# Kernel tuning notes

Hardware: AMD Instinct MI355X
Metric: run time of the kernel (lower is better)

The kernel has to match this reference:

```python
import jax, jax.numpy as jnp
import numpy as np

B, C, S, H, NC = 256, 2000, 50, 64, 3


def setup_inputs() -> dict:
    key = jax.random.key(0)
    ks = jax.random.split(key, 7)
    s = 1.0 / np.sqrt(H)  # PyTorch LSTM init scale
    return {
        "x": jax.random.normal(ks[0], (B, C, S), dtype=jnp.float32),
        "W_ih": jax.random.uniform(ks[1], (4 * H, 1), jnp.float32, -s, s),
        "W_hh": jax.random.uniform(ks[2], (4 * H, H), jnp.float32, -s, s),
        "b_ih": jax.random.uniform(ks[3], (4 * H,), jnp.float32, -s, s),
        "b_hh": jax.random.uniform(ks[4], (4 * H,), jnp.float32, -s, s),
        "W_fc": jax.random.uniform(ks[5], (NC, H), jnp.float32, -s, s),
        "b_fc": jax.random.uniform(ks[6], (NC,), jnp.float32, -s, s),
    }


def _lstm_last_h(x_flat, W_ih, W_hh, b_ih, b_hh):
    # x_flat: [N, S, 1] with N = B*C. PyTorch gate order: i, f, g, o.
    N = x_flat.shape[0]
    b = b_ih + b_hh  # [4H]
    # input_dim == 1, so precompute the input contribution for all steps:
    # [N, S, 1] @ [1, 4H] -> [N, S, 4H], then scan over time axis.
    x_proj = x_flat @ W_ih.T + b  # [N, S, 4H]
    xs = jnp.moveaxis(x_proj, 1, 0)  # [S, N, 4H]

    def step(carry, x_t):
        h, c = carry
        gates = x_t + h @ W_hh.T  # [N, 4H]
        i, f, g, o = jnp.split(gates, 4, axis=-1)
        i = jax.nn.sigmoid(i)
        f = jax.nn.sigmoid(f)
        g = jnp.tanh(g)
        o = jax.nn.sigmoid(o)
        c = f * c + i * g
        h = o * jnp.tanh(c)
        return (h, c), None

    h0 = jnp.zeros((N, x_proj.shape[-1] // 4), x_flat.dtype)
    (h_last, _), _ = jax.lax.scan(step, (h0, h0), xs)
    return h_last  # [N, H]


def reference(x, W_ih, W_hh, b_ih, b_hh, W_fc, b_fc):
    Bsz, Nc, Sl = x.shape
    x_flat = x.reshape(Bsz * Nc, Sl, 1)
    h_last = _lstm_last_h(x_flat, W_ih, W_hh, b_ih, b_hh)  # [B*C, H]
    logits = h_last @ W_fc.T + b_fc  # [B*C, NC]
    return logits.reshape(Bsz, Nc, -1)
```

## Files before the change

kernel.cpp:

```cpp
#include <hip/hip_runtime.h>

typedef _Float16 h4 __attribute__((ext_vector_type(4)));
typedef float f4 __attribute__((ext_vector_type(4)));

#define SEQ_LEN 50
#define HID 64
#define FSTRIDE 68

#if __has_builtin(__builtin_amdgcn_exp2f)
#define EXP2(x) __builtin_amdgcn_exp2f(x)
#else
extern "C" __device__ float __ocml_native_exp2_f32(float);
#define EXP2(x) __ocml_native_exp2_f32(x)
#endif
#define RCP(x) __builtin_amdgcn_rcpf(x)

#define MFMA16(A,B,C) __builtin_amdgcn_mfma_f32_16x16x16f16(A, B, C, 0, 0, 0)

#define LOG2E  1.442695041f
#define LOG2E2 2.885390082f

__global__ __launch_bounds__(256, 3)
void lstm_fused(const float* __restrict__ x,
                const float* __restrict__ W_ih,
                const float* __restrict__ W_hh,
                const float* __restrict__ b_ih,
                const float* __restrict__ b_hh,
                const float* __restrict__ W_fc,
                const float* __restrict__ b_fc,
                float* __restrict__ out)
{
    __shared__ h4    sW[16 * 4 * 64];
    __shared__ float sXT[SEQ_LEN * 64];

    const int tid  = threadIdx.x;
    const int wave = tid >> 6;
    const int lane = tid & 63;
    const int col  = lane & 15;
    const int quad = lane >> 4;
    const int seqBase = blockIdx.x << 6;

    for (int i = tid; i < SEQ_LEN * 64; i += 256) {
        const int s = i / SEQ_LEN;
        const int t = i - s * SEQ_LEN;
        sXT[t * 64 + s] = x[(size_t)(seqBase + s) * SEQ_LEN + t];
    }

    for (int i = tid; i < 16 * 4 * 64; i += 256) {
        const int ln   = i & 63;
        const int slot = (i >> 6) & 3;
        const int tile = i >> 8;
        const int gi = tile >> 2, dq = tile & 3;
        const int cl = ln & 15, qd = ln >> 4;
        const int n  = gi * 64 + dq * 16 + cl;
        const float scale = (gi == 2) ? LOG2E2 : LOG2E;
        h4 a = {};
        if (slot < 3) {
            const float* wp = W_hh + (size_t)n * HID + (slot + 1) * 16 + qd * 4;
            f4 w = *(const f4*)wp;
            a[0] = (_Float16)(w[0] * scale);
            a[1] = (_Float16)(w[1] * scale);
            a[2] = (_Float16)(w[2] * scale);
            a[3] = (_Float16)(w[3] * scale);
        } else if (qd == 0) {
            a[0] = (_Float16)(W_ih[n] * scale);
            a[1] = (_Float16)((b_ih[n] + b_hh[n]) * scale);
        }
        sW[(tile * 4 + slot) * 64 + ln] = a;
    }

    h4 Aw0[4][4];
    #pragma unroll
    for (int gi = 0; gi < 4; ++gi) {
        const float scale = (gi == 2) ? LOG2E2 : LOG2E;
        #pragma unroll
        for (int dq = 0; dq < 4; ++dq) {
            const int n = gi * 64 + dq * 16 + col;
            const float* wp = W_hh + (size_t)n * HID + quad * 4;
            f4 w = *(const f4*)wp;
            h4 a;
            a[0] = (_Float16)(w[0] * scale);
            a[1] = (_Float16)(w[1] * scale);
            a[2] = (_Float16)(w[2] * scale);
            a[3] = (_Float16)(w[3] * scale);
            Aw0[gi][dq] = a;
        }
    }

    const f4 z4 = {0.0f, 0.0f, 0.0f, 0.0f};

    h4 hB[4] = {};
    float c[4][4];
    #pragma unroll
    for (int dq = 0; dq < 4; ++dq)
        #pragma unroll
        for (int r = 0; r < 4; ++r) c[dq][r] = 0.0f;

    __syncthreads();

    #pragma clang loop unroll(disable)
    for (int t = 0; t < SEQ_LEN; ++t) {
        #pragma unroll
        for (int gi = 0; gi < 4; ++gi)
            #pragma unroll
            for (int dq = 0; dq < 4; ++dq)
                asm volatile("" : "+v"(Aw0[gi][dq]));
        int ob = lane;
        asm volatile("" : "+v"(ob));

        const float xt = sXT[t * 64 + wave * 16 + col];
        h4 bext = {};
        bext[0] = (_Float16)xt;
        bext[1] = (_Float16)1.0f;

        h4 hN[4];
        #pragma unroll
        for (int dq = 0; dq < 4; ++dq) {
            f4 acc[4];
            #pragma unroll
            for (int gi = 0; gi < 4; ++gi) {
                const int tb = (gi * 4 + dq) * 256;
                h4 ax = sW[tb + 3 * 64 + ob];
                h4 w1 = sW[tb + 0 * 64 + ob];
                h4 w2 = sW[tb + 1 * 64 + ob];
                h4 w3 = sW[tb + 2 * 64 + ob];
                f4 a = MFMA16(ax, bext, z4);
                a = MFMA16(Aw0[gi][dq], hB[0], a);
                a = MFMA16(w1, hB[1], a);
                a = MFMA16(w2, hB[2], a);
                a = MFMA16(w3, hB[3], a);
                acc[gi] = a;
            }
            h4 hv;
            #pragma unroll
            for (int rp = 0; rp < 2; ++rp) {
                const int r0 = rp * 2, r1 = r0 + 1;
                float EiA = EXP2(-acc[0][r0]);
                float EfA = EXP2(-acc[1][r0]);
                float EgA = EXP2( acc[2][r0]);
                float EoA = EXP2(-acc[3][r0]);
                float EiB = EXP2(-acc[0][r1]);
                float EfB = EXP2(-acc[1][r1]);
                float EgB = EXP2( acc[2][r1]);
                float EoB = EXP2(-acc[3][r1]);
                float piA = 1.0f + EiA, pfA = 1.0f + EfA;
                float pgA = 1.0f + EgA, poA = 1.0f + EoA;
                float piB = 1.0f + EiB, pfB = 1.0f + EfB;
                float pgB = 1.0f + EgB, poB = 1.0f + EoB;
                float t1A = piA * pgA,  t1B = piB * pgB;
                float DA  = pfA * t1A,  DB  = pfB * t1B;
                float vA  = fmaf(EgA, pfA, -pfA) * LOG2E2;
                float vB  = fmaf(EgB, pfB, -pfB) * LOG2E2;
                float numA = fmaf(c[dq][r0], t1A, vA);
                float numB = fmaf(c[dq][r1], t1B, vB);
                float R   = RCP(DA * DB);
                float cnA = fminf(numA * (R * DB), 40.0f);
                float cnB = fminf(numB * (R * DA), 40.0f);
                c[dq][r0] = cnA;
                c[dq][r1] = cnB;
                float EcA = EXP2(cnA), EcB = EXP2(cnB);
                float DhA = fmaf(poA, EcA, poA);
                float DhB = fmaf(poB, EcB, poB);
                float R2  = RCP(DhA * DhB);
                float rhA = R2 * DhB,  rhB = R2 * DhA;
                hv[r0] = (_Float16)fmaf(EcA, rhA, -rhA);
                hv[r1] = (_Float16)fmaf(EcB, rhB, -rhB);
            }
            hN[dq] = hv;
        }
        #pragma unroll
        for (int dq = 0; dq < 4; ++dq) hB[dq] = hN[dq];
    }

    __syncthreads();
    _Float16* sF = (_Float16*)sXT;
    #pragma unroll
    for (int dq = 0; dq < 4; ++dq)
        *(h4*)(sF + (wave * 16 + col) * FSTRIDE + dq * 16 + quad * 4) = hB[dq];

    if (lane < 48) {
        const int sl = lane / 3;
        const int nc = lane % 3;
        const _Float16* hp = sF + (wave * 16 + sl) * FSTRIDE;
        float a = b_fc[nc];
        #pragma unroll
        for (int u = 0; u < HID; ++u)
            a = fmaf((float)hp[u], W_fc[nc * HID + u], a);
        out[(size_t)(seqBase + wave * 16 + sl) * 3 + nc] = a;
    }
}

extern "C" void kernel_launch(void* const* d_in, const int* in_sizes, int n_in,
                              void* d_out, int out_size, void* d_ws, size_t ws_size,
                              hipStream_t stream) {
    const float* x    = (const float*)d_in[0];
    const float* W_ih = (const float*)d_in[1];
    const float* W_hh = (const float*)d_in[2];
    const float* b_ih = (const float*)d_in[3];
    const float* b_hh = (const float*)d_in[4];
    const float* W_fc = (const float*)d_in[5];
    const float* b_fc = (const float*)d_in[6];
    float* out = (float*)d_out;

    const int nSeq   = in_sizes[0] / SEQ_LEN;
    const int blocks = nSeq / 64;

    hipLaunchKernelGGL(lstm_fused, dim3(blocks), dim3(256), 0, stream,
                       x, W_ih, W_hh, b_ih, b_hh, W_fc, b_fc, out);
}
```

Measured before the change: 1.994 ms.

## Move second W_hh slice to registers and shrink LDS for higher occupancy

Keeps two of the four W_hh k-slices in registers instead of one, so each step reads only two weight fragments per tile from LDS. The input-projection weights become a packed 256-entry table masked per quad, and x is stored as fp16, which cuts LDS from about 45KB to about 23KB. Launch bounds go from 3 to 4 blocks per SIMD to raise occupancy. The final FC stage gets a rotated, unpadded read pattern to avoid bank conflicts. In exchange register pressure rises and could spill at the stricter occupancy target.

```diff
diff --git a/kernel.cpp b/kernel.cpp
--- a/kernel.cpp
+++ b/kernel.cpp
@@ -5,7 +5,6 @@
 
 #define SEQ_LEN 50
 #define HID 64
-#define FSTRIDE 68
 
 #if __has_builtin(__builtin_amdgcn_exp2f)
 #define EXP2(x) __builtin_amdgcn_exp2f(x)
@@ -20,7 +19,7 @@
 #define LOG2E  1.442695041f
 #define LOG2E2 2.885390082f
 
-__global__ __launch_bounds__(256, 3)
+__global__ __launch_bounds__(256, 4)
 void lstm_fused(const float* __restrict__ x,
                 const float* __restrict__ W_ih,
                 const float* __restrict__ W_hh,
@@ -30,8 +29,9 @@
                 const float* __restrict__ b_fc,
                 float* __restrict__ out)
 {
-    __shared__ h4    sW[16 * 4 * 64];
-    __shared__ float sXT[SEQ_LEN * 64];
+    __shared__ h4       sW[16 * 2 * 64];
+    __shared__ _Float16 sXh[SEQ_LEN * 64];
+    __shared__ unsigned sXpk[16 * 16];
 
     const int tid  = threadIdx.x;
     const int wave = tid >> 6;
@@ -43,33 +43,38 @@
     for (int i = tid; i < SEQ_LEN * 64; i += 256) {
         const int s = i / SEQ_LEN;
         const int t = i - s * SEQ_LEN;
-        sXT[t * 64 + s] = x[(size_t)(seqBase + s) * SEQ_LEN + t];
-    }
-
-    for (int i = tid; i < 16 * 4 * 64; i += 256) {
+        sXh[t * 64 + s] = (_Float16)x[(size_t)(seqBase + s) * SEQ_LEN + t];
+    }
+
+    for (int i = tid; i < 16 * 2 * 64; i += 256) {
         const int ln   = i & 63;
-        const int slot = (i >> 6) & 3;
-        const int tile = i >> 8;
+        const int s2   = (i >> 6) & 1;
+        const int tile = i >> 7;
         const int gi = tile >> 2, dq = tile & 3;
         const int cl = ln & 15, qd = ln >> 4;
         const int n  = gi * 64 + dq * 16 + cl;
         const float scale = (gi == 2) ? LOG2E2 : LOG2E;
-        h4 a = {};
-        if (slot < 3) {
-            const float* wp = W_hh + (size_t)n * HID + (slot + 1) * 16 + qd * 4;
-            f4 w = *(const f4*)wp;
-            a[0] = (_Float16)(w[0] * scale);
-            a[1] = (_Float16)(w[1] * scale);
-            a[2] = (_Float16)(w[2] * scale);
-            a[3] = (_Float16)(w[3] * scale);
-        } else if (qd == 0) {
-            a[0] = (_Float16)(W_ih[n] * scale);
-            a[1] = (_Float16)((b_ih[n] + b_hh[n]) * scale);
-        }
-        sW[(tile * 4 + slot) * 64 + ln] = a;
-    }
-
-    h4 Aw0[4][4];
+        const float* wp = W_hh + (size_t)n * HID + (s2 + 2) * 16 + qd * 4;
+        f4 w = *(const f4*)wp;
+        h4 a;
+        a[0] = (_Float16)(w[0] * scale);
+        a[1] = (_Float16)(w[1] * scale);
+        a[2] = (_Float16)(w[2] * scale);
+        a[3] = (_Float16)(w[3] * scale);
+        sW[i] = a;
+    }
+    if (tid < 256) {
+        const int cl = tid & 15, tile = tid >> 4;
+        const int gi = tile >> 2, dq = tile & 3;
+        const int n  = gi * 64 + dq * 16 + cl;
+        const float scale = (gi == 2) ? LOG2E2 : LOG2E;
+        union { _Float16 h[2]; unsigned u; } p;
+        p.h[0] = (_Float16)(W_ih[n] * scale);
+        p.h[1] = (_Float16)((b_ih[n] + b_hh[n]) * scale);
+        sXpk[tid] = p.u;
+    }
+
+    h4 Aw0[4][4], Aw1[4][4];
     #pragma unroll
     for (int gi = 0; gi < 4; ++gi) {
         const float scale = (gi == 2) ? LOG2E2 : LOG2E;
@@ -77,17 +82,20 @@
         for (int dq = 0; dq < 4; ++dq) {
             const int n = gi * 64 + dq * 16 + col;
             const float* wp = W_hh + (size_t)n * HID + quad * 4;
-            f4 w = *(const f4*)wp;
-            h4 a;
-            a[0] = (_Float16)(w[0] * scale);
-            a[1] = (_Float16)(w[1] * scale);
-            a[2] = (_Float16)(w[2] * scale);
-            a[3] = (_Float16)(w[3] * scale);
-            Aw0[gi][dq] = a;
+            f4 w0 = *(const f4*)wp;
+            f4 w1 = *(const f4*)(wp + 16);
+            h4 a0, a1;
+            a0[0] = (_Float16)(w0[0] * scale); a0[1] = (_Float16)(w0[1] * scale);
+            a0[2] = (_Float16)(w0[2] * scale); a0[3] = (_Float16)(w0[3] * scale);
+            a1[0] = (_Float16)(w1[0] * scale); a1[1] = (_Float16)(w1[1] * scale);
+            a1[2] = (_Float16)(w1[2] * scale); a1[3] = (_Float16)(w1[3] * scale);
+            Aw0[gi][dq] = a0;
+            Aw1[gi][dq] = a1;
         }
     }
 
     const f4 z4 = {0.0f, 0.0f, 0.0f, 0.0f};
+    const unsigned qmask = (quad == 0) ? 0xFFFFFFFFu : 0u;
 
     h4 hB[4] = {};
     float c[4][4];
@@ -103,14 +111,16 @@
         #pragma unroll
         for (int gi = 0; gi < 4; ++gi)
             #pragma unroll
-            for (int dq = 0; dq < 4; ++dq)
+            for (int dq = 0; dq < 4; ++dq) {
                 asm volatile("" : "+v"(Aw0[gi][dq]));
+                asm volatile("" : "+v"(Aw1[gi][dq]));
+            }
         int ob = lane;
         asm volatile("" : "+v"(ob));
-
-        const float xt = sXT[t * 64 + wave * 16 + col];
+        const int obc = ob & 15;
+
         h4 bext = {};
-        bext[0] = (_Float16)xt;
+        bext[0] = sXh[t * 64 + wave * 16 + col];
         bext[1] = (_Float16)1.0f;
 
         h4 hN[4];
@@ -119,14 +129,15 @@
             f4 acc[4];
             #pragma unroll
             for (int gi = 0; gi < 4; ++gi) {
-                const int tb = (gi * 4 + dq) * 256;
-                h4 ax = sW[tb + 3 * 64 + ob];
-                h4 w1 = sW[tb + 0 * 64 + ob];
-                h4 w2 = sW[tb + 1 * 64 + ob];
-                h4 w3 = sW[tb + 2 * 64 + ob];
-                f4 a = MFMA16(ax, bext, z4);
+                const int tile = gi * 4 + dq;
+                union { unsigned u2[2]; h4 v; } axc;
+                axc.u2[0] = sXpk[tile * 16 + obc] & qmask;
+                axc.u2[1] = 0u;
+                h4 w2 = sW[(tile * 2 + 0) * 64 + ob];
+                h4 w3 = sW[(tile * 2 + 1) * 64 + ob];
+                f4 a = MFMA16(axc.v, bext, z4);
                 a = MFMA16(Aw0[gi][dq], hB[0], a);
-                a = MFMA16(w1, hB[1], a);
+                a = MFMA16(Aw1[gi][dq], hB[1], a);
                 a = MFMA16(w2, hB[2], a);
                 a = MFMA16(w3, hB[3], a);
                 acc[gi] = a;
@@ -173,19 +184,22 @@
     }
 
     __syncthreads();
-    _Float16* sF = (_Float16*)sXT;
+    _Float16* sF = (_Float16*)sW;
     #pragma unroll
     for (int dq = 0; dq < 4; ++dq)
-        *(h4*)(sF + (wave * 16 + col) * FSTRIDE + dq * 16 + quad * 4) = hB[dq];
+        *(h4*)(sF + (wave * 16 + col) * HID + dq * 16 + quad * 4) = hB[dq];
 
     if (lane < 48) {
         const int sl = lane / 3;
         const int nc = lane % 3;
-        const _Float16* hp = sF + (wave * 16 + sl) * FSTRIDE;
+        const _Float16* hp = sF + (wave * 16 + sl) * HID;
         float a = b_fc[nc];
-        #pragma unroll
-        for (int u = 0; u < HID; ++u)
+        const int u0 = (sl * 4) & 63;
+        #pragma unroll
+        for (int k = 0; k < HID; ++k) {
+            const int u = (u0 + k) & 63;
             a = fmaf((float)hp[u], W_fc[nc * HID + u], a);
+        }
         out[(size_t)(seqBase + wave * 16 + sl) * 3 + nc] = a;
     }
 }
```

Measured after the change: 2.114 ms. 1.06x slower.
